# Kernel tuning notes

Measured on AMD Instinct MI355X. Metric: run time of the kernel, lower is better.

The kernel has to match this reference:

```python
import jax, jax.numpy as jnp
import numpy as np

N1 = 128      # neurons_1
N2 = 128      # neurons_2
K = 8         # num_cluster
G = 1000      # number of graphs
NPG = 500     # nodes per graph
N = G * NPG   # total nodes
NEG_SLOPE = 0.45


def setup_inputs() -> dict:
    key = jax.random.key(0)
    ks = jax.random.split(key, 5)
    x = jax.random.normal(ks[0], (N, N1), dtype=jnp.float32)
    cls = jax.random.randint(ks[1], (N,), 0, K, dtype=jnp.int32)
    batch = jnp.repeat(jnp.arange(G, dtype=jnp.int32), NPG)  # sorted graph ids
    W1 = jax.random.normal(ks[2], (N1, N2), dtype=jnp.float32) * 0.05
    b1 = jnp.zeros((N2,), dtype=jnp.float32)
    Wa = jax.random.normal(ks[3], (N2, 1), dtype=jnp.float32) * 0.05
    ba = jnp.zeros((1,), dtype=jnp.float32)
    return {"x": x, "W1": W1, "b1": b1, "Wa": Wa, "ba": ba, "cls": cls, "batch": batch}


def reference(x, W1, b1, Wa, ba, cls, batch):
    # ---- unpooling_featurizer, cluster_method='fixed' (GI-M2), vectorized ----
    # composite segment id: one segment per (graph, cluster)
    seg = batch.astype(jnp.int32) * K + cls.astype(jnp.int32)          # [N]
    csum = jax.ops.segment_sum(x, seg, num_segments=G * K)             # [G*K, N1]
    counts = jax.ops.segment_sum(jnp.ones((N,), jnp.float32), seg,
                                 num_segments=G * K)                   # [G*K]
    # fixed: random_sets == cls, so gather each node's own cluster sum.
    # ratio_i = counts[cls_i]/Ng, renormalized over graph -> counts[cls_i]/sum_k counts_k^2
    cnode = counts[seg]                                                # [N]
    denom = jax.ops.segment_sum(cnode, batch, num_segments=G)          # [G] = sum_k c_k^2
    ratio = cnode / denom[batch]                                       # [N]
    r_x = csum[seg] * ratio[:, None]                                   # [N, N1]
    # ---- attention MLP ----
    h = jax.nn.leaky_relu(r_x @ W1 + b1, negative_slope=NEG_SLOPE)     # [N, N2]
    logits = (h @ Wa + ba)[:, 0]                                       # [N]
    # ---- segment softmax over graphs ----
    m = jax.ops.segment_max(logits, batch, num_segments=G)             # [G]
    z = jnp.exp(logits - m[batch])
    s = jax.ops.segment_sum(z, batch, num_segments=G)
    return (z / s[batch])[:, None]                                     # [N, 1]
```

## Files before the change

### kernel.cpp

```cpp
#include <hip/hip_runtime.h>

#define GG 1000
#define NPG 500
#define KK 8
#define N1 128
#define N2 128
#define NEG_SLOPE 0.45f
#define NTHREADS 512
#define NWAVES 8
#define CHUNK ((NPG + NWAVES - 1) / NWAVES)

__global__ __launch_bounds__(NTHREADS) void cluster_attn_kernel(
    const float* __restrict__ x,
    const float* __restrict__ W1,
    const float* __restrict__ b1,
    const float* __restrict__ Wa,
    const float* __restrict__ ba,
    const int*   __restrict__ cls,
    float*       __restrict__ out)
{
    __shared__ float s_acc[KK][N1];
    __shared__ float s_hw[KK * N2];
    __shared__ int   s_cls[NPG];
    __shared__ int   s_order[NPG];
    __shared__ int   s_wcnt[NWAVES][KK];
    __shared__ int   s_start[KK];
    __shared__ float s_fcnt[KK];
    __shared__ float s_ratio[KK];
    __shared__ float s_L[KK];
    __shared__ float s_e[KK];

    const int g   = blockIdx.x;
    const int tid = threadIdx.x;
    const int w   = tid >> 6;
    const int l   = tid & 63;

    const int* clsg = cls + (size_t)g * NPG;
    float* accf = &s_acc[0][0];
    for (int i = tid; i < KK * N1; i += NTHREADS) accf[i] = 0.f;

    int myc = -1;
    if (tid < NPG) { myc = clsg[tid]; s_cls[tid] = myc; }

    unsigned long long mymask = 0;
    #pragma unroll
    for (int k = 0; k < KK; ++k) {
        unsigned long long m = __ballot(myc == k);
        if (l == 0) s_wcnt[w][k] = (int)__popcll(m);
        if (myc == k) mymask = m;
    }
    __syncthreads();

    if (tid == 0) {
        int run = 0; float d = 0.f;
        #pragma unroll
        for (int k = 0; k < KK; ++k) {
            int t = 0;
            #pragma unroll
            for (int ww = 0; ww < NWAVES; ++ww) t += s_wcnt[ww][k];
            s_start[k] = run; run += t;
            float c = (float)t; s_fcnt[k] = c; d += c * c;
        }
        #pragma unroll
        for (int k = 0; k < KK; ++k) s_ratio[k] = s_fcnt[k] / d;
    }
    __syncthreads();

    if (tid < NPG) {
        int before = 0;
        for (int ww = 0; ww < w; ++ww) before += s_wcnt[ww][myc];
        before += (int)__popcll(mymask & ((1ULL << l) - 1ULL));
        s_order[s_start[myc] + before] = tid | (myc << 12);
    }
    __syncthreads();

    const float2* x2 = (const float2*)(x + (size_t)g * NPG * N1);
    {
        int begin = w * CHUNK;
        int end   = begin + CHUNK; if (end > NPG) end = NPG;
        if (begin < end) {
            int cur = __builtin_amdgcn_readfirstlane(s_order[begin]) >> 12;
            float a0 = 0.f, a1 = 0.f;
            int e = begin;

#define STEP(P, V)                                                      \
            {                                                           \
                int c_ = (P) >> 12;                                     \
                if (c_ != cur) {                \
                    atomicAdd(&s_acc[cur][2 * l],     a0);              \
                    atomicAdd(&s_acc[cur][2 * l + 1], a1);              \
                    a0 = 0.f; a1 = 0.f; cur = c_;                       \
                }                                                       \
                a0 += (V).x; a1 += (V).y;                               \
            }

            for (; e + 4 <= end; e += 4) {
                int p0 = __builtin_amdgcn_readfirstlane(s_order[e]);
                int p1 = __builtin_amdgcn_readfirstlane(s_order[e + 1]);
                int p2 = __builtin_amdgcn_readfirstlane(s_order[e + 2]);
                int p3 = __builtin_amdgcn_readfirstlane(s_order[e + 3]);
                float2 v0 = x2[(size_t)(p0 & 0xFFF) * 64 + l];
                float2 v1 = x2[(size_t)(p1 & 0xFFF) * 64 + l];
                float2 v2 = x2[(size_t)(p2 & 0xFFF) * 64 + l];
                float2 v3 = x2[(size_t)(p3 & 0xFFF) * 64 + l];
                STEP(p0, v0) STEP(p1, v1) STEP(p2, v2) STEP(p3, v3)
            }
            for (; e < end; ++e) {
                int p = __builtin_amdgcn_readfirstlane(s_order[e]);
                float2 v = x2[(size_t)(p & 0xFFF) * 64 + l];
                STEP(p, v)
            }
#undef STEP
            atomicAdd(&s_acc[cur][2 * l],     a0);
            atomicAdd(&s_acc[cur][2 * l + 1], a1);
        }
    }
    __syncthreads();

    #pragma unroll
    for (int r = 0; r < 2; ++r) {
        int idx = tid + r * NTHREADS;
        int k = idx >> 7;
        int j = idx & 127;
        float s = 0.f;
        #pragma unroll 4
        for (int f = 0; f < N1; ++f)
            s = fmaf(accf[k * N1 + f], W1[f * N2 + j], s);
        float val = fmaf(s, s_ratio[k], b1[j]);
        float h = val > 0.f ? val : NEG_SLOPE * val;
        s_hw[idx] = h * Wa[j];
    }
    __syncthreads();

    {
        float v = s_hw[w * 128 + l] + s_hw[w * 128 + 64 + l];
        #pragma unroll
        for (int off = 32; off > 0; off >>= 1) v += __shfl_down(v, off);
        if (l == 0) s_L[w] = v + ba[0];
    }
    __syncthreads();

    if (tid == 0) {
        float m = -1e30f;
        #pragma unroll
        for (int k = 0; k < KK; ++k)
            if (s_fcnt[k] > 0.f) m = fmaxf(m, s_L[k]);
        float ssum = 0.f;
        float ek[KK];
        #pragma unroll
        for (int k = 0; k < KK; ++k) {
            ek[k] = (s_fcnt[k] > 0.f) ? expf(s_L[k] - m) : 0.f;
            ssum += s_fcnt[k] * ek[k];
        }
        #pragma unroll
        for (int k = 0; k < KK; ++k) s_e[k] = ek[k] / ssum;
    }
    __syncthreads();

    float* outg = out + (size_t)g * NPG;
    for (int n = tid; n < NPG; n += NTHREADS) outg[n] = s_e[s_cls[n]];
}

extern "C" void kernel_launch(void* const* d_in, const int* in_sizes, int n_in,
                              void* d_out, int out_size, void* d_ws, size_t ws_size,
                              hipStream_t stream) {
    const float* x   = (const float*)d_in[0];
    const float* W1  = (const float*)d_in[1];
    const float* b1  = (const float*)d_in[2];
    const float* Wa  = (const float*)d_in[3];
    const float* ba  = (const float*)d_in[4];
    const int*   cls = (const int*)d_in[5];

    float* out = (float*)d_out;
    cluster_attn_kernel<<<GG, NTHREADS, 0, stream>>>(x, W1, b1, Wa, ba, cls, out);
}
```

Baseline: 59.64 us.

## Split each wave into two half-waves loading float4 rows from two node streams

Each wave's 64 sorted node entries are now held in a register and split between two half-waves, each reading a different node row with 16-byte float4 loads instead of 8-byte float2 loads. Sort order is padded to 512 entries, and the padding maps to a dummy ninth accumulator cluster. This aims to widen memory transactions and keep more loads in flight per wave. It adds lane-divergent flush branches and more LDS atomics per flush.

```diff
diff --git a/kernel.cpp b/kernel.cpp
--- a/kernel.cpp
+++ b/kernel.cpp
@@ -8,7 +8,6 @@
 #define NEG_SLOPE 0.45f
 #define NTHREADS 512
 #define NWAVES 8
-#define CHUNK ((NPG + NWAVES - 1) / NWAVES)
 
 __global__ __launch_bounds__(NTHREADS) void cluster_attn_kernel(
     const float* __restrict__ x,
@@ -19,10 +18,10 @@
     const int*   __restrict__ cls,
     float*       __restrict__ out)
 {
-    __shared__ float s_acc[KK][N1];
+    __shared__ float s_acc[KK + 1][N1];
     __shared__ float s_hw[KK * N2];
     __shared__ int   s_cls[NPG];
-    __shared__ int   s_order[NPG];
+    __shared__ int   s_order[NTHREADS];
     __shared__ int   s_wcnt[NWAVES][KK];
     __shared__ int   s_start[KK];
     __shared__ float s_fcnt[KK];
@@ -34,10 +33,12 @@
     const int tid = threadIdx.x;
     const int w   = tid >> 6;
     const int l   = tid & 63;
+    const bool hi = l >= 32;
+    const int qb  = (l & 31) * 16;
 
     const int* clsg = cls + (size_t)g * NPG;
     float* accf = &s_acc[0][0];
-    for (int i = tid; i < KK * N1; i += NTHREADS) accf[i] = 0.f;
+    for (int i = tid; i < (KK + 1) * N1; i += NTHREADS) accf[i] = 0.f;
 
     int myc = -1;
     if (tid < NPG) { myc = clsg[tid]; s_cls[tid] = myc; }
@@ -71,50 +72,50 @@
         for (int ww = 0; ww < w; ++ww) before += s_wcnt[ww][myc];
         before += (int)__popcll(mymask & ((1ULL << l) - 1ULL));
         s_order[s_start[myc] + before] = tid | (myc << 12);
+    } else {
+        s_order[tid] = 0 | (8 << 12);
     }
     __syncthreads();
 
-    const float2* x2 = (const float2*)(x + (size_t)g * NPG * N1);
-    {
-        int begin = w * CHUNK;
-        int end   = begin + CHUNK; if (end > NPG) end = NPG;
-        if (begin < end) {
-            int cur = __builtin_amdgcn_readfirstlane(s_order[begin]) >> 12;
-            float a0 = 0.f, a1 = 0.f;
-            int e = begin;
+    const int ordreg = s_order[(w << 6) | l];
+    const char* xrow = (const char*)(x + (size_t)g * NPG * N1);
 
-#define STEP(P, V)                                                      \
-            {                                                           \
-                int c_ = (P) >> 12;                                     \
-                if (c_ != cur) {                \
-                    atomicAdd(&s_acc[cur][2 * l],     a0);              \
-                    atomicAdd(&s_acc[cur][2 * l + 1], a1);              \
-                    a0 = 0.f; a1 = 0.f; cur = c_;                       \
-                }                                                       \
-                a0 += (V).x; a1 += (V).y;                               \
-            }
+    float a0 = 0.f, a1 = 0.f, a2 = 0.f, a3 = 0.f;
+    int cur0 = __builtin_amdgcn_readlane(ordreg, 0)  >> 12;
+    int cur1 = __builtin_amdgcn_readlane(ordreg, 32) >> 12;
 
-            for (; e + 4 <= end; e += 4) {
-                int p0 = __builtin_amdgcn_readfirstlane(s_order[e]);
-                int p1 = __builtin_amdgcn_readfirstlane(s_order[e + 1]);
-                int p2 = __builtin_amdgcn_readfirstlane(s_order[e + 2]);
-                int p3 = __builtin_amdgcn_readfirstlane(s_order[e + 3]);
-                float2 v0 = x2[(size_t)(p0 & 0xFFF) * 64 + l];
-                float2 v1 = x2[(size_t)(p1 & 0xFFF) * 64 + l];
-                float2 v2 = x2[(size_t)(p2 & 0xFFF) * 64 + l];
-                float2 v3 = x2[(size_t)(p3 & 0xFFF) * 64 + l];
-                STEP(p0, v0) STEP(p1, v1) STEP(p2, v2) STEP(p3, v3)
-            }
-            for (; e < end; ++e) {
-                int p = __builtin_amdgcn_readfirstlane(s_order[e]);
-                float2 v = x2[(size_t)(p & 0xFFF) * 64 + l];
-                STEP(p, v)
-            }
-#undef STEP
-            atomicAdd(&s_acc[cur][2 * l],     a0);
-            atomicAdd(&s_acc[cur][2 * l + 1], a1);
-        }
+#define FLUSH(C)                                                         \
+    {                                                                    \
+        atomicAdd(&s_acc[C][(l & 31) * 4 + 0], a0);                      \
+        atomicAdd(&s_acc[C][(l & 31) * 4 + 1], a1);                      \
+        atomicAdd(&s_acc[C][(l & 31) * 4 + 2], a2);                      \
+        atomicAdd(&s_acc[C][(l & 31) * 4 + 3], a3);                      \
+        a0 = 0.f; a1 = 0.f; a2 = 0.f; a3 = 0.f;                          \
     }
+#define LOADP(P, E)                                                      \
+    const int olo##P = __builtin_amdgcn_readlane(ordreg, (E));           \
+    const int ohi##P = __builtin_amdgcn_readlane(ordreg, 32 + (E));      \
+    const int nd##P  = hi ? (ohi##P & 0xFFF) : (olo##P & 0xFFF);         \
+    const float4 v##P = *(const float4*)(xrow + ((size_t)nd##P << 9) + qb);
+#define PROC(P)                                                          \
+    {                                                                    \
+        const int clo = olo##P >> 12, chi = ohi##P >> 12;                \
+        if (clo != cur0) { if (!hi) FLUSH(cur0); cur0 = clo; }           \
+        if (chi != cur1) { if (hi)  FLUSH(cur1); cur1 = chi; }           \
+        a0 += v##P.x; a1 += v##P.y; a2 += v##P.z; a3 += v##P.w;          \
+    }
+
+    #pragma unroll 2
+    for (int it = 0; it < 8; ++it) {
+        const int e = it * 4;
+        LOADP(0, e) LOADP(1, e + 1) LOADP(2, e + 2) LOADP(3, e + 3)
+        PROC(0) PROC(1) PROC(2) PROC(3)
+    }
+    if (!hi) FLUSH(cur0);
+    if (hi)  FLUSH(cur1);
+#undef PROC
+#undef LOADP
+#undef FLUSH
     __syncthreads();
 
     #pragma unroll
```

Result: slower. 61.51 us (+3.1%).

## Restructure cluster MLP to reuse each W1 load across all clusters

Applied to the files above, without the earlier changes.

The per-graph 8x128 by 128x128 matvec is reorganised so each thread owns one output column and a quarter of the input features. It reads each W1 element once and applies it to all 8 cluster rows. Partial sums are reduced with lane shuffles, and the Wa projection is reduced in-wave, which removes the s_hw shared buffer and one barrier. The cost is more registers and shuffle traffic, plus a cross-wave sum of the partial logits done by thread 0.

```diff
diff --git a/kernel.cpp b/kernel.cpp
--- a/kernel.cpp
+++ b/kernel.cpp
@@ -20,14 +20,13 @@
     float*       __restrict__ out)
 {
     __shared__ float s_acc[KK][N1];
-    __shared__ float s_hw[KK * N2];
     __shared__ int   s_cls[NPG];
     __shared__ int   s_order[NPG];
     __shared__ int   s_wcnt[NWAVES][KK];
     __shared__ int   s_start[KK];
+    __shared__ float s_Lp[NWAVES][KK];
     __shared__ float s_fcnt[KK];
     __shared__ float s_ratio[KK];
-    __shared__ float s_L[KK];
     __shared__ float s_e[KK];
 
     const int g   = blockIdx.x;
@@ -117,39 +116,59 @@
     }
     __syncthreads();
 
-    #pragma unroll
-    for (int r = 0; r < 2; ++r) {
-        int idx = tid + r * NTHREADS;
-        int k = idx >> 7;
-        int j = idx & 127;
-        float s = 0.f;
+    {
+        const int   jt  = (w << 4) + (l & 15);
+        const int   fg  = l >> 4;
+        const float b1j = b1[jt];
+        const float Waj = Wa[jt];
+        float p[KK];
+        #pragma unroll
+        for (int k = 0; k < KK; ++k) p[k] = 0.f;
+
+        const float* w1p = W1 + (size_t)(fg * 32) * N2 + jt;
         #pragma unroll 4
-        for (int f = 0; f < N1; ++f)
-            s = fmaf(accf[k * N1 + f], W1[f * N2 + j], s);
-        float val = fmaf(s, s_ratio[k], b1[j]);
-        float h = val > 0.f ? val : NEG_SLOPE * val;
-        s_hw[idx] = h * Wa[j];
-    }
-    __syncthreads();
-
-    {
-        float v = s_hw[w * 128 + l] + s_hw[w * 128 + 64 + l];
+        for (int i = 0; i < 32; ++i) {
+            const float wv = w1p[(size_t)i * N2];
+            const int   f  = fg * 32 + i;
+            #pragma unroll
+            for (int k = 0; k < KK; ++k)
+                p[k] = fmaf(accf[k * N1 + f], wv, p[k]);
+        }
         #pragma unroll
-        for (int off = 32; off > 0; off >>= 1) v += __shfl_down(v, off);
-        if (l == 0) s_L[w] = v + ba[0];
+        for (int k = 0; k < KK; ++k) {
+            float v = p[k];
+            v += __shfl_xor(v, 16);
+            v += __shfl_xor(v, 32);
+            float val = fmaf(v, s_ratio[k], b1j);
+            float h = val > 0.f ? val : NEG_SLOPE * val;
+            float c = h * Waj;
+            c += __shfl_xor(c, 1);
+            c += __shfl_xor(c, 2);
+            c += __shfl_xor(c, 4);
+            c += __shfl_xor(c, 8);
+            if (l == 0) s_Lp[w][k] = c;
+        }
     }
     __syncthreads();
 
     if (tid == 0) {
+        float Lk[KK];
+        #pragma unroll
+        for (int k = 0; k < KK; ++k) {
+            float s = ba[0];
+            #pragma unroll
+            for (int ww = 0; ww < NWAVES; ++ww) s += s_Lp[ww][k];
+            Lk[k] = s;
+        }
         float m = -1e30f;
         #pragma unroll
         for (int k = 0; k < KK; ++k)
-            if (s_fcnt[k] > 0.f) m = fmaxf(m, s_L[k]);
+            if (s_fcnt[k] > 0.f) m = fmaxf(m, Lk[k]);
         float ssum = 0.f;
         float ek[KK];
         #pragma unroll
         for (int k = 0; k < KK; ++k) {
-            ek[k] = (s_fcnt[k] > 0.f) ? expf(s_L[k] - m) : 0.f;
+            ek[k] = (s_fcnt[k] > 0.f) ? expf(Lk[k] - m) : 0.f;
             ssum += s_fcnt[k] * ek[k];
         }
         #pragma unroll
```

New measurement: 55.32 us. 7.2% less time.
